# Kernel optimization log

Measured on AMD Instinct MI355X. Metric: run time of the kernel, lower is better.

The kernel has to match this reference:

```python
import jax, jax.numpy as jnp
import numpy as np

DIM = 2048
HEADS = 16
DIM_HEAD = 128
ROPE_THETA = 10000.0


def _rope(t):
    # t: [b, h, n, d]; lucidrains rotary-embedding-torch style (interleaved pairs)
    n, d = t.shape[-2], t.shape[-1]
    inv_freq = 1.0 / (ROPE_THETA ** (jnp.arange(0, d, 2, dtype=jnp.float32) / d))  # [d/2]
    freqs = jnp.arange(n, dtype=jnp.float32)[:, None] * inv_freq[None, :]          # [n, d/2]
    freqs = jnp.repeat(freqs, 2, axis=-1)                                          # [n, d]
    cos, sin = jnp.cos(freqs), jnp.sin(freqs)
    x1 = t[..., 0::2]
    x2 = t[..., 1::2]
    rot = jnp.stack((-x2, x1), axis=-1).reshape(t.shape)  # rotate_half on interleaved pairs
    return t * cos + rot * sin


def setup_inputs() -> dict:
    key = jax.random.key(0)
    k1, k2, k3 = jax.random.split(key, 3)
    x = jax.random.normal(k1, (2, 2048, DIM), dtype=jnp.float32)
    gamma = jnp.ones((DIM,), dtype=jnp.float32)
    w_qkv = jax.random.normal(k2, (DIM, 3 * HEADS * DIM_HEAD), dtype=jnp.float32) * 0.02
    w_out = jax.random.normal(k3, (HEADS * DIM_HEAD, DIM), dtype=jnp.float32) * 0.02
    return {"x": x, "gamma": gamma, "w_qkv": w_qkv, "w_out": w_out}


def reference(x, gamma, w_qkv, w_out):
    b, n, dim = x.shape
    # RMSNorm: F.normalize(x, dim=-1) * sqrt(dim) * gamma
    norm = jnp.linalg.norm(x, axis=-1, keepdims=True)
    xn = x / jnp.maximum(norm, 1e-12) * (dim ** 0.5) * gamma
    # QKV projection; 'b n (qkv h d) -> qkv b h n d'
    qkv = (xn @ w_qkv).reshape(b, n, 3, HEADS, DIM_HEAD).transpose(2, 0, 3, 1, 4)
    q, k, v = qkv[0], qkv[1], qkv[2]
    cached_kv = jnp.stack((k, v))  # [2, b, h, n, d] (pre-RoPE, as in original)
    q = _rope(q)
    k = _rope(k)
    sim = jnp.einsum('bhid,bhjd->bhij', q, k) * (DIM_HEAD ** -0.5)
    causal_mask = jnp.triu(jnp.ones((n, n), dtype=bool), 1)
    sim = jnp.where(causal_mask, -jnp.finfo(sim.dtype).max, sim)
    attn = jax.nn.softmax(sim, axis=-1)
    out = jnp.einsum('bhij,bhjd->bhid', attn, v)
    out = out.transpose(0, 2, 1, 3).reshape(b, n, HEADS * DIM_HEAD)
    out = out @ w_out
    return (out, cached_kv)
```

## Files before the change

### kernel.cpp

```cpp
#include <hip/hip_runtime.h>
#include <cstdint>
#include <cstddef>
#include <math.h>

#define SEQ   2048
#define DIM   2048
#define NQKV  6144
#define NH    16
#define DH    128
#define ROWS  4096

typedef unsigned short u16;
typedef unsigned int u32;
typedef __attribute__((ext_vector_type(8))) short bf16x8;
typedef __attribute__((ext_vector_type(4))) float f32x4;
typedef __attribute__((ext_vector_type(16))) float f32x16;

__device__ __forceinline__ u16 f2bf(float f) {
  union { float f; u32 u; } v;
  v.f = f;
  u32 r = v.u + 0x7FFFu + ((v.u >> 16) & 1u);
  return (u16)(r >> 16);
}

__device__ __forceinline__ void gll16(const u16* g, u16* l) {
  __builtin_amdgcn_global_load_lds(
      (const __attribute__((address_space(1))) u32*)(const void*)g,
      (__attribute__((address_space(3))) u32*)(void*)l,
      16, 0, 0);
}

__global__ __launch_bounds__(64) void rms_bf16(
    const float* __restrict__ x, const float* __restrict__ g,
    u16* __restrict__ xnb) {
  int row = blockIdx.x, lane = threadIdx.x;
  const float* xr = x + (size_t)row * DIM;
  double ss = 0.0;
  for (int c = lane; c < DIM; c += 64) { double v = xr[c]; ss += v * v; }
  #pragma unroll
  for (int off = 32; off >= 1; off >>= 1) ss += __shfl_xor(ss, off);
  double nrm = sqrt(ss); if (nrm < 1e-12) nrm = 1e-12;
  double sc = 45.254833995939045 / nrm;
  u16* dst = xnb + (size_t)row * DIM;
  for (int c = lane; c < DIM; c += 64)
    dst[c] = f2bf((float)((double)xr[c] * sc * (double)g[c]));
}

__global__ void transpose_f32_bf16(const float* __restrict__ in,
                                   u16* __restrict__ out, int R, int C) {
  __shared__ float tile[32][33];
  int bx = blockIdx.x * 32;
  int by = blockIdx.y * 32;
  int tx = threadIdx.x, ty = threadIdx.y;
  #pragma unroll
  for (int j = 0; j < 32; j += 8)
    tile[ty + j][tx] = in[(size_t)(by + ty + j) * C + bx + tx];
  __syncthreads();
  #pragma unroll
  for (int j = 0; j < 32; j += 8)
    out[(size_t)(bx + ty + j) * R + by + tx] = f2bf(tile[tx][ty + j]);
}

__global__ __launch_bounds__(256) void rope_table(float2* __restrict__ tab) {
  int gid = blockIdx.x * 256 + threadIdx.x;
  int p = gid & 63;
  int n = gid >> 6;
  double inv = pow(10000.0, -(double)p / 64.0);
  double ang = (double)n * inv;
  tab[gid] = make_float2((float)cos(ang), (float)sin(ang));
}

__global__ __launch_bounds__(256) void gemm_nt(
    const u16* __restrict__ A, const u16* __restrict__ BT,
    float* __restrict__ C, int M, int N, int K) {
  __shared__ u16 As[128 * 32];
  __shared__ u16 Bs[128 * 32];
  int nbn = N >> 7;
  int chunk = nbn >> 3;
  int wg = blockIdx.x;
  int xcd = wg & 7, g = wg >> 3;
  int bm = (g / chunk) * 128;
  int bn = (xcd * chunk + g % chunk) * 128;

  int tid = threadIdx.x;
  int wid = tid >> 6, lane = tid & 63;
  int wr = wid >> 1, wc = wid & 1;
  int fr = lane & 15, fq = lane >> 4;
  int srow_hi = lane >> 2;
  int scol = (lane & 3) * 8;

  f32x4 acc[4][4] = {};

  const u16* a_rd = As + (wr * 64 + fr) * 32 + fq * 8;
  const u16* b_rd = Bs + (wc * 64 + fr) * 32 + fq * 8;

  for (int k0 = 0; k0 < K; k0 += 32) {
    __syncthreads();
    #pragma unroll
    for (int i = 0; i < 2; ++i) {
      int c = wid * 2 + i;
      int row = c * 16 + srow_hi;
      gll16(A  + (size_t)(bm + row) * K + k0 + scol, As + c * 512);
      gll16(BT + (size_t)(bn + row) * K + k0 + scol, Bs + c * 512);
    }
    __syncthreads();

    bf16x8 af[4], bfr[4];
    #pragma unroll
    for (int m = 0; m < 4; ++m) af[m]  = *(const bf16x8*)(a_rd + m * 16 * 32);
    #pragma unroll
    for (int n = 0; n < 4; ++n) bfr[n] = *(const bf16x8*)(b_rd + n * 16 * 32);
    #pragma unroll
    for (int m = 0; m < 4; ++m)
      #pragma unroll
      for (int n = 0; n < 4; ++n)
        acc[m][n] = __builtin_amdgcn_mfma_f32_16x16x32_bf16(af[m], bfr[n], acc[m][n], 0, 0, 0);
  }
  #pragma unroll
  for (int m = 0; m < 4; ++m)
    #pragma unroll
    for (int n = 0; n < 4; ++n)
      #pragma unroll
      for (int r = 0; r < 4; ++r) {
        int row = bm + wr * 64 + m * 16 + fq * 4 + r;
        int col = bn + wc * 64 + n * 16 + fr;
        C[(size_t)row * N + col] = acc[m][n][r];
      }
}

__global__ __launch_bounds__(256) void gemm_qkv(
    const u16* __restrict__ A, const u16* __restrict__ BT,
    float* __restrict__ cached, u16* __restrict__ qpk,
    float* __restrict__ vbuf, const float2* __restrict__ tab) {
  const int M = ROWS, N = NQKV, K = DIM;
  __shared__ u16 As[128 * 32];
  __shared__ u16 Bs[128 * 32];
  int nbn = N >> 7;
  int chunk = nbn >> 3;
  int wg = blockIdx.x;
  int xcd = wg & 7, g = wg >> 3;
  int bm = (g / chunk) * 128;
  int bn = (xcd * chunk + g % chunk) * 128;

  int tid = threadIdx.x;
  int wid = tid >> 6, lane = tid & 63;
  int wr = wid >> 1, wc = wid & 1;
  int fr = lane & 15, fq = lane >> 4;
  int srow_hi = lane >> 2;
  int scol = (lane & 3) * 8;

  f32x4 acc[4][4] = {};

  const u16* a_rd = As + (wr * 64 + fr) * 32 + fq * 8;
  const u16* b_rd = Bs + (wc * 64 + fr) * 32 + fq * 8;

  for (int k0 = 0; k0 < K; k0 += 32) {
    __syncthreads();
    #pragma unroll
    for (int i = 0; i < 2; ++i) {
      int c = wid * 2 + i;
      int row = c * 16 + srow_hi;
      gll16(A  + (size_t)(bm + row) * K + k0 + scol, As + c * 512);
      gll16(BT + (size_t)(bn + row) * K + k0 + scol, Bs + c * 512);
    }
    __syncthreads();

    bf16x8 af[4], bfr[4];
    #pragma unroll
    for (int m = 0; m < 4; ++m) af[m]  = *(const bf16x8*)(a_rd + m * 16 * 32);
    #pragma unroll
    for (int n = 0; n < 4; ++n) bfr[n] = *(const bf16x8*)(b_rd + n * 16 * 32);
    #pragma unroll
    for (int m = 0; m < 4; ++m)
      #pragma unroll
      for (int n = 0; n < 4; ++n)
        acc[m][n] = __builtin_amdgcn_mfma_f32_16x16x32_bf16(af[m], bfr[n], acc[m][n], 0, 0, 0);
  }

  int typ = bn >> 11;
  if (typ < 2) {
    #pragma unroll
    for (int m = 0; m < 4; ++m)
      #pragma unroll
      for (int nn = 0; nn < 4; ++nn)
        #pragma unroll
        for (int r = 0; r < 4; ++r) {
          int gr = bm + wr * 64 + m * 16 + fq * 4 + r;
          int gc = bn + wc * 64 + nn * 16 + fr;
          int n = gr & 2047;
          int lc = gc & 2047;
          int d = lc & 127;
          float v = acc[m][nn][r];
          float w = __shfl_xor(v, 1);
          float2 cs = tab[n * 64 + (d >> 1)];
          float o = (d & 1) ? (v * cs.x + w * cs.y) : (v * cs.x - w * cs.y);
          qpk[(size_t)gr * 4096 + typ * 2048 + lc] = f2bf(o);
          if (typ == 1) {
            int b = gr >> 11, h = lc >> 7;
            cached[((size_t)(b * NH + h) * SEQ + n) * DH + d] = v;
          }
        }
  } else {
    #pragma unroll
    for (int m = 0; m < 4; ++m)
      #pragma unroll
      for (int nn = 0; nn < 4; ++nn)
        #pragma unroll
        for (int r = 0; r < 4; ++r) {
          int gr = bm + wr * 64 + m * 16 + fq * 4 + r;
          int gc = bn + wc * 64 + nn * 16 + fr;
          int n = gr & 2047, b = gr >> 11;
          int lc = gc - 4096;
          int d = lc & 127, h = lc >> 7;
          float v = acc[m][nn][r];
          cached[8388608 + ((size_t)(b * NH + h) * SEQ + n) * DH + d] = v;
          vbuf[(size_t)gr * 2048 + lc] = v;
        }
  }
}

__global__ void transpose_v_cast(const float* __restrict__ vbuf,
                                 u16* __restrict__ vT) {
  int bh = blockIdx.z; int b = bh >> 4, h = bh & 15;
  int d0 = blockIdx.x * 32, n0 = blockIdx.y * 32;
  __shared__ float tile[32][33];
  int tx = threadIdx.x, ty = threadIdx.y;
  const float* src = vbuf + (size_t)(b * SEQ + n0) * 2048 + h * DH + d0;
  #pragma unroll
  for (int j = 0; j < 32; j += 8)
    tile[ty + j][tx] = src[(size_t)(ty + j) * 2048 + tx];
  __syncthreads();
  u16* dst = vT + ((size_t)bh * DH + d0) * SEQ + n0;
  #pragma unroll
  for (int j = 0; j < 32; j += 8)
    dst[(size_t)(ty + j) * SEQ + tx] = f2bf(tile[tx][ty + j]);
}

__global__ __launch_bounds__(64) void attn_swap(
    const u16* __restrict__ qkp,
    const u16* __restrict__ vT,
    u16* __restrict__ ctx) {
  int wg = blockIdx.x;
  int xcd = wg & 7;
  int g   = wg >> 3;
  int bh  = (g >> 5) * 8 + xcd;
  int qp  = g & 31;
  int b = bh >> 4, h = bh & 15;
  int lane = threadIdx.x;
  int ln = lane & 31;
  int hi = lane >> 5;

  const size_t rstr = 4096;
  const u16* Qb = qkp + (size_t)(b * SEQ) * rstr + h * 128;
  const u16* Kb = Qb + 2048;
  const u16* Vt = vT + (size_t)bh * DH * SEQ;
  const float scale = 0.08838834764831845f;

  #pragma unroll 1
  for (int ph = 0; ph < 2; ++ph) {
    int qt = ph ? (63 - qp) : qp;
    int qr0 = qt * 32;
    int q_own = qr0 + ln;

    bf16x8 qf[8];
    {
      const u16* qrow = Qb + (size_t)q_own * rstr + hi * 8;
      #pragma unroll
      for (int kc = 0; kc < 8; ++kc) qf[kc] = *(const bf16x8*)(qrow + kc * 16);
    }

    f32x16 acc[4] = {};
    float m = -3e38f, l = 0.f;

    bf16x8 kreg[8];
    {
      const u16* krow = Kb + (size_t)ln * rstr + hi * 8;
      #pragma unroll
      for (int kc = 0; kc < 8; ++kc) kreg[kc] = *(const bf16x8*)(krow + kc * 16);
    }

    for (int jt = 0; jt <= qt; ++jt) {
      int j0 = jt * 32;

      bf16x8 vfrag[8];
      #pragma unroll
      for (int t = 0; t < 2; ++t)
        #pragma unroll
        for (int db = 0; db < 4; ++db)
          vfrag[t * 4 + db] =
              *(const bf16x8*)(Vt + (size_t)(db * 32 + ln) * SEQ + j0 + t * 16 + hi * 8);

      f32x16 sacc0 = {}, sacc1 = {};
      __builtin_amdgcn_s_setprio(1);
      #pragma unroll
      for (int kc = 0; kc < 4; ++kc)
        sacc0 = __builtin_amdgcn_mfma_f32_32x32x16_bf16(kreg[kc], qf[kc], sacc0, 0, 0, 0);
      #pragma unroll
      for (int kc = 4; kc < 8; ++kc)
        sacc1 = __builtin_amdgcn_mfma_f32_32x32x16_bf16(kreg[kc], qf[kc], sacc1, 0, 0, 0);
      __builtin_amdgcn_s_setprio(0);
      f32x16 sacc = sacc0 + sacc1;

      if (jt < qt) {
        const u16* krow = Kb + (size_t)(j0 + 32 + ln) * rstr + hi * 8;
        #pragma unroll
        for (int kc = 0; kc < 8; ++kc) kreg[kc] = *(const bf16x8*)(krow + kc * 16);
      }

      float p[16];
      #pragma unroll
      for (int r = 0; r < 16; ++r) {
        int kv = j0 + (r & 3) + 8 * (r >> 2) + 4 * hi;
        float v = sacc[r] * scale;
        p[r] = (kv > q_own) ? -1e30f : v;
      }

      float t8[8];
      #pragma unroll
      for (int i = 0; i < 8; ++i) t8[i] = fmaxf(p[i], p[i + 8]);
      #pragma unroll
      for (int i = 0; i < 4; ++i) t8[i] = fmaxf(t8[i], t8[i + 4]);
      float mx = fmaxf(fmaxf(t8[0], t8[1]), fmaxf(t8[2], t8[3]));
      mx = fmaxf(mx, __shfl_xor(mx, 32));

      if (!__all(mx - m <= 8.f)) {
        float mn = fmaxf(m, mx);
        float al = __expf(m - mn);
        m = mn;
        l *= al;
        #pragma unroll
        for (int r = 0; r < 16; ++r) {
          float alr = __shfl(al, (r & 3) + 8 * (r >> 2) + 4 * hi);
          #pragma unroll
          for (int db = 0; db < 4; ++db) acc[db][r] *= alr;
        }
      }

      #pragma unroll
      for (int r = 0; r < 16; ++r) p[r] = __expf(p[r] - m);
      float s8[8];
      #pragma unroll
      for (int i = 0; i < 8; ++i) s8[i] = p[i] + p[i + 8];
      #pragma unroll
      for (int i = 0; i < 4; ++i) s8[i] = s8[i] + s8[i + 4];
      float sum = (s8[0] + s8[1]) + (s8[2] + s8[3]);
      sum += __shfl_xor(sum, 32);
      l += sum;

      u32 pk[8], swk[8];
      #pragma unroll
      for (int i = 0; i < 8; ++i)
        pk[i] = (u32)f2bf(p[2 * i]) | ((u32)f2bf(p[2 * i + 1]) << 16);
      #pragma unroll
      for (int i = 0; i < 8; ++i) swk[i] = __shfl_xor(pk[i], 32);

      union { u32 w[4]; bf16x8 v; } pf0, pf1;
      pf0.w[0] = hi ? swk[2] : pk[0];
      pf0.w[1] = hi ? swk[3] : pk[1];
      pf0.w[2] = hi ? pk[2]  : swk[0];
      pf0.w[3] = hi ? pk[3]  : swk[1];
      pf1.w[0] = hi ? swk[6] : pk[4];
      pf1.w[1] = hi ? swk[7] : pk[5];
      pf1.w[2] = hi ? pk[6]  : swk[4];
      pf1.w[3] = hi ? pk[7]  : swk[5];

      __builtin_amdgcn_s_setprio(1);
      #pragma unroll
      for (int db = 0; db < 4; ++db) {
        acc[db] = __builtin_amdgcn_mfma_f32_32x32x16_bf16(pf0.v, vfrag[db],     acc[db], 0, 0, 0);
        acc[db] = __builtin_amdgcn_mfma_f32_32x32x16_bf16(pf1.v, vfrag[4 + db], acc[db], 0, 0, 0);
      }
      __builtin_amdgcn_s_setprio(0);
    }

    float linv = 1.f / l;
    #pragma unroll
    for (int r = 0; r < 16; ++r) {
      int qrow = (r & 3) + 8 * (r >> 2) + 4 * hi;
      float lr = __shfl(linv, qrow);
      int q = qr0 + qrow;
      u16* crow = ctx + (size_t)(b * SEQ + q) * DIM + h * DH + ln;
      #pragma unroll
      for (int db = 0; db < 4; ++db)
        crow[db * 32] = f2bf(acc[db][r] * lr);
    }
  }
}

extern "C" void kernel_launch(void* const* d_in, const int* in_sizes, int n_in,
                              void* d_out, int out_size, void* d_ws, size_t ws_size,
                              hipStream_t stream) {
  const float *x = nullptr, *gamma = nullptr, *wq = nullptr, *wo = nullptr;
  for (int ii = 0; ii < n_in; ++ii) {
    switch (in_sizes[ii]) {
      case  8388608: x     = (const float*)d_in[ii]; break;
      case     2048: gamma = (const float*)d_in[ii]; break;
      case 12582912: wq    = (const float*)d_in[ii]; break;
      case  4194304: wo    = (const float*)d_in[ii]; break;
    }
  }
  if (!x || !gamma || !wq || !wo) {
    x = (const float*)d_in[0]; gamma = (const float*)d_in[1];
    wq = (const float*)d_in[2]; wo = (const float*)d_in[3];
  }

  float* out    = (float*)d_out;
  float* cached = out + 8388608;

  char* ws = (char*)d_ws;
  u16*   xnb   = (u16*)ws;
  u16*   qpk   = (u16*)(ws + 16777216);
  float* vbuf  = (float*)(ws + 50331648);
  u16*   wqkvT = (u16*)(ws + 83886080);
  u16*   woutT = (u16*)(ws + 109051904);
  u16*   ctx   = (u16*)(ws + 117440512);
  u16*   vT    = (u16*)d_out;
  float2* tab  = (float2*)((char*)d_out + 16777216);

  rms_bf16<<<ROWS, 64, 0, stream>>>(x, gamma, xnb);
  rope_table<<<131072 / 256, 256, 0, stream>>>(tab);
  transpose_f32_bf16<<<dim3(NQKV / 32, DIM / 32), dim3(32, 8), 0, stream>>>(wq, wqkvT, DIM, NQKV);
  transpose_f32_bf16<<<dim3(DIM / 32, DIM / 32), dim3(32, 8), 0, stream>>>(wo, woutT, DIM, DIM);
  gemm_qkv<<<(ROWS / 128) * (NQKV / 128), 256, 0, stream>>>(xnb, wqkvT, cached, qpk, vbuf, tab);
  transpose_v_cast<<<dim3(DH / 32, SEQ / 32, 32), dim3(32, 8), 0, stream>>>(vbuf, vT);
  attn_swap<<<1024, 64, 0, stream>>>(qpk, vT, ctx);
  gemm_nt<<<(ROWS / 128) * (DIM / 128), 256, 0, stream>>>(ctx, woutT, out, ROWS, DIM, DIM);
}
```

Before: 414.1 us.

## Split attention KV loop across two waves and store V buffer as bf16

The attention kernel now launches two waves per workgroup. Each wave processes half of the causal KV tiles, and the partial softmax states are merged through shared memory using the max/sum rescaling. This doubles the active waves per query tile and shortens the serial KV loop. Separately, the QKV GEMM writes the V staging buffer in bf16 instead of fp32, which halves the traffic for the transpose kernel. The trade-offs are extra LDS use (about 17KB per block), two barriers per phase, and a merge step done by only one wave.

Result: no change. 417.4 us (+0.8%).

```diff
diff --git a/kernel.cpp b/kernel.cpp
--- a/kernel.cpp
+++ b/kernel.cpp
@@ -131,7 +131,7 @@
 __global__ __launch_bounds__(256) void gemm_qkv(
     const u16* __restrict__ A, const u16* __restrict__ BT,
     float* __restrict__ cached, u16* __restrict__ qpk,
-    float* __restrict__ vbuf, const float2* __restrict__ tab) {
+    u16* __restrict__ vbuf, const float2* __restrict__ tab) {
   const int M = ROWS, N = NQKV, K = DIM;
   __shared__ u16 As[128 * 32];
   __shared__ u16 Bs[128 * 32];
@@ -214,18 +214,18 @@
           int d = lc & 127, h = lc >> 7;
           float v = acc[m][nn][r];
           cached[8388608 + ((size_t)(b * NH + h) * SEQ + n) * DH + d] = v;
-          vbuf[(size_t)gr * 2048 + lc] = v;
+          vbuf[(size_t)gr * 2048 + lc] = f2bf(v);
         }
   }
 }
 
-__global__ void transpose_v_cast(const float* __restrict__ vbuf,
+__global__ void transpose_v_bf16(const u16* __restrict__ vbuf,
                                  u16* __restrict__ vT) {
   int bh = blockIdx.z; int b = bh >> 4, h = bh & 15;
   int d0 = blockIdx.x * 32, n0 = blockIdx.y * 32;
-  __shared__ float tile[32][33];
+  __shared__ u16 tile[32][34];
   int tx = threadIdx.x, ty = threadIdx.y;
-  const float* src = vbuf + (size_t)(b * SEQ + n0) * 2048 + h * DH + d0;
+  const u16* src = vbuf + (size_t)(b * SEQ + n0) * 2048 + h * DH + d0;
   #pragma unroll
   for (int j = 0; j < 32; j += 8)
     tile[ty + j][tx] = src[(size_t)(ty + j) * 2048 + tx];
@@ -233,10 +233,10 @@
   u16* dst = vT + ((size_t)bh * DH + d0) * SEQ + n0;
   #pragma unroll
   for (int j = 0; j < 32; j += 8)
-    dst[(size_t)(ty + j) * SEQ + tx] = f2bf(tile[tx][ty + j]);
-}
-
-__global__ __launch_bounds__(64) void attn_swap(
+    dst[(size_t)(ty + j) * SEQ + tx] = tile[tx][ty + j];
+}
+
+__global__ __launch_bounds__(128) void attn_swap(
     const u16* __restrict__ qkp,
     const u16* __restrict__ vT,
     u16* __restrict__ ctx) {
@@ -246,9 +246,14 @@
   int bh  = (g >> 5) * 8 + xcd;
   int qp  = g & 31;
   int b = bh >> 4, h = bh & 15;
-  int lane = threadIdx.x;
+  int tid = threadIdx.x;
+  int wv = tid >> 6;
+  int lane = tid & 63;
   int ln = lane & 31;
   int hi = lane >> 5;
+
+  __shared__ float accbuf[64][65];
+  __shared__ float mbuf[64], lbuf[64];
 
   const size_t rstr = 4096;
   const u16* Qb = qkp + (size_t)(b * SEQ) * rstr + h * 128;
@@ -261,6 +266,10 @@
     int qt = ph ? (63 - qp) : qp;
     int qr0 = qt * 32;
     int q_own = qr0 + ln;
+    int ntile = qt + 1;
+    int half = (ntile + 1) >> 1;
+    int ks0 = wv ? half : 0;
+    int ks1 = wv ? ntile : half;
 
     bf16x8 qf[8];
     {
@@ -274,12 +283,12 @@
 
     bf16x8 kreg[8];
     {
-      const u16* krow = Kb + (size_t)ln * rstr + hi * 8;
+      const u16* krow = Kb + (size_t)(ks0 * 32 + ln) * rstr + hi * 8;
       #pragma unroll
       for (int kc = 0; kc < 8; ++kc) kreg[kc] = *(const bf16x8*)(krow + kc * 16);
     }
 
-    for (int jt = 0; jt <= qt; ++jt) {
+    for (int jt = ks0; jt < ks1; ++jt) {
       int j0 = jt * 32;
 
       bf16x8 vfrag[8];
@@ -301,7 +310,7 @@
       __builtin_amdgcn_s_setprio(0);
       f32x16 sacc = sacc0 + sacc1;
 
-      if (jt < qt) {
+      if (jt + 1 < ks1) {
         const u16* krow = Kb + (size_t)(j0 + 32 + ln) * rstr + hi * 8;
         #pragma unroll
         for (int kc = 0; kc < 8; ++kc) kreg[kc] = *(const bf16x8*)(krow + kc * 16);
@@ -373,17 +382,38 @@
       __builtin_amdgcn_s_setprio(0);
     }
 
-    float linv = 1.f / l;
-    #pragma unroll
-    for (int r = 0; r < 16; ++r) {
-      int qrow = (r & 3) + 8 * (r >> 2) + 4 * hi;
-      float lr = __shfl(linv, qrow);
-      int q = qr0 + qrow;
-      u16* crow = ctx + (size_t)(b * SEQ + q) * DIM + h * DH + ln;
+    if (wv == 1) {
+      mbuf[lane] = m;
+      lbuf[lane] = l;
       #pragma unroll
       for (int db = 0; db < 4; ++db)
-        crow[db * 32] = f2bf(acc[db][r] * lr);
-    }
+        #pragma unroll
+        for (int r = 0; r < 16; ++r)
+          accbuf[lane][db * 16 + r] = acc[db][r];
+    }
+    __syncthreads();
+    if (wv == 0) {
+      float mB = mbuf[lane], lB = lbuf[lane];
+      float mM = fmaxf(m, mB);
+      float eA = __expf(m - mM);
+      float eB = __expf(mB - mM);
+      float linv = 1.f / (l * eA + lB * eB);
+      #pragma unroll
+      for (int r = 0; r < 16; ++r) {
+        int qrow = (r & 3) + 8 * (r >> 2) + 4 * hi;
+        float eAr = __shfl(eA, qrow);
+        float eBr = __shfl(eB, qrow);
+        float lr  = __shfl(linv, qrow);
+        int q = qr0 + qrow;
+        u16* crow = ctx + (size_t)(b * SEQ + q) * DIM + h * DH + ln;
+        #pragma unroll
+        for (int db = 0; db < 4; ++db) {
+          float o = acc[db][r] * eAr + accbuf[lane][db * 16 + r] * eBr;
+          crow[db * 32] = f2bf(o * lr);
+        }
+      }
+    }
+    __syncthreads();
   }
 }
 
@@ -410,7 +440,7 @@
   char* ws = (char*)d_ws;
   u16*   xnb   = (u16*)ws;
   u16*   qpk   = (u16*)(ws + 16777216);
-  float* vbuf  = (float*)(ws + 50331648);
+  u16*   vbuf  = (u16*)(ws + 50331648);
   u16*   wqkvT = (u16*)(ws + 83886080);
   u16*   woutT = (u16*)(ws + 109051904);
   u16*   ctx   = (u16*)(ws + 117440512);
@@ -422,7 +452,7 @@
   transpose_f32_bf16<<<dim3(NQKV / 32, DIM / 32), dim3(32, 8), 0, stream>>>(wq, wqkvT, DIM, NQKV);
   transpose_f32_bf16<<<dim3(DIM / 32, DIM / 32), dim3(32, 8), 0, stream>>>(wo, woutT, DIM, DIM);
   gemm_qkv<<<(ROWS / 128) * (NQKV / 128), 256, 0, stream>>>(xnb, wqkvT, cached, qpk, vbuf, tab);
-  transpose_v_cast<<<dim3(DH / 32, SEQ / 32, 32), dim3(32, 8), 0, stream>>>(vbuf, vT);
-  attn_swap<<<1024, 64, 0, stream>>>(qpk, vT, ctx);
+  transpose_v_bf16<<<dim3(DH / 32, SEQ / 32, 32), dim3(32, 8), 0, stream>>>(vbuf, vT);
+  attn_swap<<<1024, 128, 0, stream>>>(qpk, vT, ctx);
   gemm_nt<<<(ROWS / 128) * (DIM / 128), 256, 0, stream>>>(ctx, woutT, out, ROWS, DIM, DIM);
 }
```
